# Kernel optimization log

Hardware: AMD Instinct MI355X
Metric: run time of the kernel (lower is better)

Reference implementation:

```python
import jax, jax.numpy as jnp
import numpy as np

N_NODES = 100000


def gcn_conv(x, src, dst, W, b, n_nodes):
    # PyG GCNConv: h = X W; out[i] = sum_j norm_ij * h[j] + b, with self-loops
    # and symmetric normalization norm_ij = deg(i)^-1/2 * deg(j)^-1/2.
    h = x @ W  # [N, out]
    deg = jax.ops.segment_sum(jnp.ones_like(dst, dtype=h.dtype), dst, num_segments=n_nodes)
    dinv = jnp.where(deg > 0, jax.lax.rsqrt(deg), 0.0)
    norm = dinv[src] * dinv[dst]  # [E]
    msg = h[src] * norm[:, None]  # [E, out] gather + scale
    out = jax.ops.segment_sum(msg, dst, num_segments=n_nodes)  # scatter-add
    return out + b


def setup_inputs() -> dict:
    key = jax.random.key(0)
    k_x, k_e, k_w1, k_w2 = jax.random.split(key, 4)
    in_c, hid, out_c = 128, 64, 32
    x = jax.random.normal(k_x, (N_NODES, in_c), dtype=jnp.float32)
    edge_index = jax.random.randint(k_e, (2, 1600000), 0, N_NODES, dtype=jnp.int32)
    W1 = jax.random.normal(k_w1, (in_c, hid), dtype=jnp.float32) / np.sqrt(in_c)
    b1 = jnp.zeros((hid,), dtype=jnp.float32)
    W2 = jax.random.normal(k_w2, (hid, out_c), dtype=jnp.float32) / np.sqrt(hid)
    b2 = jnp.zeros((out_c,), dtype=jnp.float32)
    return {"x": x, "edge_index": edge_index, "W1": W1, "b1": b1, "W2": W2, "b2": b2}


def reference(x, edge_index, W1, b1, W2, b2):
    n = x.shape[0]
    # add self-loops (GCNConv default)
    loops = jnp.arange(n, dtype=edge_index.dtype)
    src = jnp.concatenate([edge_index[0], loops])
    dst = jnp.concatenate([edge_index[1], loops])
    # faithful to original forward: x = (x*x)/x
    x = (x * x) / x
    h = jax.nn.relu(gcn_conv(x, src, dst, W1, b1, n))
    return gcn_conv(h, src, dst, W2, b2, n)
```

## Files before the change

### kernel.cpp

```cpp
#include <hip/hip_runtime.h>
#include <hip/hip_fp16.h>


#define IN_C 128
#define HID 64
#define OUTC 32
#define BSH 9
#define BSZ 512
#define EPB 8192

typedef _Float16 half8 __attribute__((ext_vector_type(8)));
typedef float f32x4 __attribute__((ext_vector_type(4)));

static __host__ __device__ __forceinline__ size_t szt(int a) { return (size_t)a; }

__global__ __launch_bounds__(256) void k_hist(const int* __restrict__ dst, int E,
                                              int* __restrict__ hist) {
  __shared__ int h[256];
  int tid = threadIdx.x;
  h[tid] = 0;
  __syncthreads();
  int e0 = blockIdx.x * EPB;
  int e1 = min(e0 + EPB, E);
  for (int i = e0 + tid; i < e1; i += 256) atomicAdd(&h[dst[i] >> BSH], 1);
  __syncthreads();
  hist[blockIdx.x * 256 + tid] = h[tid];
}

__global__ __launch_bounds__(256) void k_scan(int* __restrict__ hist, int B,
                                              int* __restrict__ bucket_base,
                                              int* __restrict__ bucket_count) {
  int k = threadIdx.x;
  int run = 0;
  int b = 0;
  for (; b + 4 <= B; b += 4) {
    int v0 = hist[(b + 0) * 256 + k];
    int v1 = hist[(b + 1) * 256 + k];
    int v2 = hist[(b + 2) * 256 + k];
    int v3 = hist[(b + 3) * 256 + k];
    hist[(b + 0) * 256 + k] = run; run += v0;
    hist[(b + 1) * 256 + k] = run; run += v1;
    hist[(b + 2) * 256 + k] = run; run += v2;
    hist[(b + 3) * 256 + k] = run; run += v3;
  }
  for (; b < B; ++b) {
    int v = hist[b * 256 + k];
    hist[b * 256 + k] = run;
    run += v;
  }
  __shared__ int sc[256];
  sc[k] = run;
  __syncthreads();
  for (int o = 1; o < 256; o <<= 1) {
    int v = (k >= o) ? sc[k - o] : 0;
    __syncthreads();
    sc[k] += v;
    __syncthreads();
  }
  bucket_base[k] = sc[k] - run;
  bucket_count[k] = run;
}

__global__ __launch_bounds__(256) void k_scatter(const int* __restrict__ src,
                                                 const int* __restrict__ dst, int E,
                                                 const int* __restrict__ hist,
                                                 const int* __restrict__ bucket_base,
                                                 int* __restrict__ bedges) {
  __shared__ int off[256];
  int tid = threadIdx.x;
  off[tid] = hist[blockIdx.x * 256 + tid] + bucket_base[tid];
  __syncthreads();
  int e0 = blockIdx.x * EPB;
  int e1 = min(e0 + EPB, E);
  for (int i = e0 + tid; i < e1; i += 256) {
    int d = dst[i], s = src[i];
    int p = atomicAdd(&off[d >> BSH], 1);
    bedges[p] = (s << BSH) | (d & (BSZ - 1));
  }
}

__global__ __launch_bounds__(256) void k_bucket(const int* __restrict__ bedges,
                                                const int* __restrict__ bucket_base,
                                                const int* __restrict__ bucket_count,
                                                int2* __restrict__ rd,
                                                float* __restrict__ dinv,
                                                int* __restrict__ csr, int N) {
  __shared__ int h[BSZ];
  __shared__ int pfx[BSZ];
  __shared__ int cnt[BSZ];
  __shared__ int sc[256];
  int tid = threadIdx.x;
  int b = blockIdx.x;
  int base = bucket_base[b];
  int nE = bucket_count[b];
  h[tid] = 0; h[tid + 256] = 0;
  cnt[tid] = 0; cnt[tid + 256] = 0;
  __syncthreads();
  for (int i = tid; i < nE; i += 256) atomicAdd(&h[bedges[base + i] & (BSZ - 1)], 1);
  __syncthreads();
  int a0 = h[2 * tid], a1 = h[2 * tid + 1];
  int s = a0 + a1;
  sc[tid] = s;
  __syncthreads();
  for (int o = 1; o < 256; o <<= 1) {
    int v = (tid >= o) ? sc[tid - o] : 0;
    __syncthreads();
    sc[tid] += v;
    __syncthreads();
  }
  int ex = sc[tid] - s;
  pfx[2 * tid] = ex;
  pfx[2 * tid + 1] = ex + a0;
  __syncthreads();
  for (int i = tid; i < BSZ; i += 256) {
    int node = b * BSZ + i;
    if (node < N) {
      int dg = h[i];
      rd[node] = make_int2(base + pfx[i], dg);
      dinv[node] = rsqrtf((float)(dg + 1));
    }
  }
  for (int i = tid; i < nE; i += 256) {
    int e = bedges[base + i];
    int l = e & (BSZ - 1);
    int p = pfx[l] + atomicAdd(&cnt[l], 1);
    csr[base + p] = e >> BSH;
  }
}

__global__ __launch_bounds__(256) void k_gemm1(
    const float* __restrict__ x, const float* __restrict__ W1,
    const float* __restrict__ dinv, __half* __restrict__ h1s, int N) {
  __shared__ _Float16 bf[4 * 4 * 64 * 8];
  const int tid = threadIdx.x;
  for (int idx = tid; idx < 128 * 64; idx += 256) {
    int k = idx >> 6, c = idx & 63;
    int kc = k >> 5, kk = k & 31;
    int chunk = kk >> 3, j = kk & 7;
    int ct = c >> 4, cl = c & 15;
    bf[(((kc * 4 + ct) * 64) + chunk * 16 + cl) * 8 + j] = (_Float16)W1[idx];
  }
  __syncthreads();

  const int lane = tid & 63, wave = tid >> 6;
  const int row0 = blockIdx.x * 64 + wave * 16;
  const int r_a = lane & 15;
  const int chk = lane >> 4;
  const int arow = min(row0 + r_a, N - 1);
  const float* xp = x + szt(arow) * IN_C + chk * 8;

  f32x4 acc[4];
  #pragma unroll
  for (int ct = 0; ct < 4; ++ct) acc[ct] = (f32x4){0.f, 0.f, 0.f, 0.f};

  #pragma unroll
  for (int kc = 0; kc < 4; ++kc) {
    float4 a0 = *reinterpret_cast<const float4*>(xp + kc * 32);
    float4 a1v = *reinterpret_cast<const float4*>(xp + kc * 32 + 4);
    half8 af;
    af[0] = (_Float16)a0.x;  af[1] = (_Float16)a0.y;
    af[2] = (_Float16)a0.z;  af[3] = (_Float16)a0.w;
    af[4] = (_Float16)a1v.x; af[5] = (_Float16)a1v.y;
    af[6] = (_Float16)a1v.z; af[7] = (_Float16)a1v.w;
    #pragma unroll
    for (int ct = 0; ct < 4; ++ct) {
      half8 bfrag = *reinterpret_cast<const half8*>(&bf[(((kc * 4 + ct) * 64) + lane) * 8]);
      acc[ct] = __builtin_amdgcn_mfma_f32_16x16x32_f16(af, bfrag, acc[ct], 0, 0, 0);
    }
  }
  #pragma unroll
  for (int r = 0; r < 4; ++r) {
    int drow = row0 + chk * 4 + r;
    if (drow < N) {
      float di = dinv[drow];
      #pragma unroll
      for (int ct = 0; ct < 4; ++ct)
        h1s[szt(drow) * HID + ct * 16 + r_a] = (__half)(acc[ct][r] * di);
    }
  }
}

__global__ __launch_bounds__(256) void k_agg1(
    const __half2* __restrict__ h1s2, const int* __restrict__ csr,
    const int2* __restrict__ rd, const float* __restrict__ dinv,
    const float2* __restrict__ b1f2, __half2* __restrict__ a1_2, int N) {
  int node = blockIdx.x * 8 + (threadIdx.x >> 5);
  if (node >= N) return;
  int l = threadIdx.x & 31;
  float2 acc = __half22float2(h1s2[szt(node) * 32 + l]);
  int2 v = rd[node];
  int base = v.x, cnt = v.y;
  if (cnt > 0) {
    int last = base + cnt - 1;
    int idx[8];
    #pragma unroll
    for (int u = 0; u < 8; ++u) idx[u] = csr[min(base + u, last)];
    for (int j = 0; j < cnt; j += 8) {
      __half2 g[8];
      #pragma unroll
      for (int u = 0; u < 8; ++u) g[u] = h1s2[szt(idx[u]) * 32 + l];
      int jn = j + 8;
      if (jn < cnt) {
        #pragma unroll
        for (int u = 0; u < 8; ++u) idx[u] = csr[min(base + jn + u, last)];
      }
      #pragma unroll
      for (int u = 0; u < 8; ++u) {
        float2 f = __half22float2(g[u]);
        bool ok = (j + u) < cnt;
        acc.x += ok ? f.x : 0.0f;
        acc.y += ok ? f.y : 0.0f;
      }
    }
  }
  float di = dinv[node];
  float2 bb = b1f2[l];
  float ox = fmaxf(di * acc.x + bb.x, 0.0f);
  float oy = fmaxf(di * acc.y + bb.y, 0.0f);
  a1_2[szt(node) * 32 + l] = __floats2half2_rn(ox, oy);
}

__global__ __launch_bounds__(256) void k_gemm2(
    const __half* __restrict__ a1, const float* __restrict__ W2,
    const float* __restrict__ dinv, __half* __restrict__ h2s, int N) {
  __shared__ _Float16 bf[2 * 2 * 64 * 8];
  const int tid = threadIdx.x;
  for (int idx = tid; idx < 64 * 32; idx += 256) {
    int k = idx >> 5, c = idx & 31;
    int kc = k >> 5, kk = k & 31;
    int chunk = kk >> 3, j = kk & 7;
    int ct = c >> 4, cl = c & 15;
    bf[(((kc * 2 + ct) * 64) + chunk * 16 + cl) * 8 + j] = (_Float16)W2[idx];
  }
  __syncthreads();

  const int lane = tid & 63, wave = tid >> 6;
  const int row0 = blockIdx.x * 64 + wave * 16;
  const int r_a = lane & 15;
  const int chk = lane >> 4;
  const int arow = min(row0 + r_a, N - 1);
  const _Float16* ap = (const _Float16*)a1 + szt(arow) * HID + chk * 8;

  f32x4 acc[2];
  acc[0] = (f32x4){0.f, 0.f, 0.f, 0.f};
  acc[1] = (f32x4){0.f, 0.f, 0.f, 0.f};
  #pragma unroll
  for (int kc = 0; kc < 2; ++kc) {
    half8 af = *reinterpret_cast<const half8*>(ap + kc * 32);
    #pragma unroll
    for (int ct = 0; ct < 2; ++ct) {
      half8 bfrag = *reinterpret_cast<const half8*>(&bf[(((kc * 2 + ct) * 64) + lane) * 8]);
      acc[ct] = __builtin_amdgcn_mfma_f32_16x16x32_f16(af, bfrag, acc[ct], 0, 0, 0);
    }
  }
  #pragma unroll
  for (int r = 0; r < 4; ++r) {
    int drow = row0 + chk * 4 + r;
    if (drow < N) {
      float di = dinv[drow];
      #pragma unroll
      for (int ct = 0; ct < 2; ++ct)
        h2s[szt(drow) * OUTC + ct * 16 + r_a] = (__half)(acc[ct][r] * di);
    }
  }
}

__global__ __launch_bounds__(256) void k_agg2(
    const __half2* __restrict__ h2s2, const int* __restrict__ csr,
    const int2* __restrict__ rd, const float* __restrict__ dinv,
    const float2* __restrict__ b2f2, float2* __restrict__ out2, int N) {
  int node = blockIdx.x * 16 + (threadIdx.x >> 4);
  if (node >= N) return;
  int l = threadIdx.x & 15;
  float2 acc = __half22float2(h2s2[szt(node) * 16 + l]);
  int2 v = rd[node];
  int base = v.x, cnt = v.y;
  if (cnt > 0) {
    int last = base + cnt - 1;
    int idx[8];
    #pragma unroll
    for (int u = 0; u < 8; ++u) idx[u] = csr[min(base + u, last)];
    for (int j = 0; j < cnt; j += 8) {
      __half2 g[8];
      #pragma unroll
      for (int u = 0; u < 8; ++u) g[u] = h2s2[szt(idx[u]) * 16 + l];
      int jn = j + 8;
      if (jn < cnt) {
        #pragma unroll
        for (int u = 0; u < 8; ++u) idx[u] = csr[min(base + jn + u, last)];
      }
      #pragma unroll
      for (int u = 0; u < 8; ++u) {
        float2 f = __half22float2(g[u]);
        bool ok = (j + u) < cnt;
        acc.x += ok ? f.x : 0.0f;
        acc.y += ok ? f.y : 0.0f;
      }
    }
  }
  float di = dinv[node];
  float2 bb = b2f2[l];
  out2[szt(node) * 16 + l] = make_float2(di * acc.x + bb.x, di * acc.y + bb.y);
}

extern "C" void kernel_launch(void* const* d_in, const int* in_sizes, int n_in,
                              void* d_out, int out_size, void* d_ws, size_t ws_size,
                              hipStream_t stream) {
  const float* x  = (const float*)d_in[0];
  const int*   ei = (const int*)d_in[1];
  const float* W1 = (const float*)d_in[2];
  const float* b1 = (const float*)d_in[3];
  const float* W2 = (const float*)d_in[4];
  const float* b2 = (const float*)d_in[5];
  float* out = (float*)d_out;

  const int N = in_sizes[0] / IN_C;
  const int E = in_sizes[1] / 2;
  const int* src = ei;
  const int* dst = ei + E;

  const int B  = (E + EPB - 1) / EPB;
  const int K1 = (N + BSZ - 1) / BSZ;

  char* ws = (char*)d_ws;
  size_t off = 0;
  auto alloc = [&](size_t bytes) {
    off = (off + 255) & ~(size_t)255;
    void* p = ws + off;
    off += bytes;
    return p;
  };
  int*    hist   = (int*)alloc(szt(B) * 256 * 4);
  int*    bbase  = (int*)alloc(256 * 4);
  int*    bcount = (int*)alloc(256 * 4);
  int2*   rd     = (int2*)alloc(szt(N) * 8);
  float*  dinv   = (float*)alloc(szt(N) * 4);
  int*    bedges = (int*)alloc(szt(E) * 4);
  int*    csr    = (int*)alloc(szt(E) * 4);
  __half* h1s    = (__half*)alloc(szt(N) * HID * 2);
  __half* a1     = (__half*)alloc(szt(N) * HID * 2);
  __half* h2s    = (__half*)alloc(szt(N) * OUTC * 2);
  (void)ws_size;

  k_hist<<<B, 256, 0, stream>>>(dst, E, hist);
  k_scan<<<1, 256, 0, stream>>>(hist, B, bbase, bcount);
  k_scatter<<<B, 256, 0, stream>>>(src, dst, E, hist, bbase, bedges);
  k_bucket<<<K1, 256, 0, stream>>>(bedges, bbase, bcount, rd, dinv, csr, N);
  k_gemm1<<<(N + 63) / 64, 256, 0, stream>>>(x, W1, dinv, h1s, N);
  k_agg1<<<(N + 7) / 8, 256, 0, stream>>>(
      (const __half2*)h1s, csr, rd, dinv, (const float2*)b1, (__half2*)a1, N);
  k_gemm2<<<(N + 63) / 64, 256, 0, stream>>>(a1, W2, dinv, h2s, N);
  k_agg2<<<(N + 15) / 16, 256, 0, stream>>>(
      (const __half2*)h2s, csr, rd, dinv, (const float2*)b2, (float2*)out, N);
}
```

Baseline: 139.5 us.

## Parallelize histogram scan and widen aggregation gathers to 16-byte vectors

Replaces the single-block serial column scan with a per-bucket parallel scan kernel plus a small base scan. Both aggregation kernels now use fewer lanes per node and load eight halves per lane, sharing neighbour indices across lanes with wave shuffles. The aim is to cut per-edge load instruction count and the serial scan latency. The new scan assumes at most 256 edge blocks, and the wider per-lane work raises register use.

```diff
diff --git a/kernel.cpp b/kernel.cpp
--- a/kernel.cpp
+++ b/kernel.cpp
@@ -7,6 +7,7 @@
 #define OUTC 32
 #define BSH 9
 #define BSZ 512
+#define NSLOT 256
 #define EPB 8192
 
 typedef _Float16 half8 __attribute__((ext_vector_type(8)));
@@ -16,7 +17,7 @@
 
 __global__ __launch_bounds__(256) void k_hist(const int* __restrict__ dst, int E,
                                               int* __restrict__ hist) {
-  __shared__ int h[256];
+  __shared__ int h[NSLOT];
   int tid = threadIdx.x;
   h[tid] = 0;
   __syncthreads();
@@ -24,41 +25,40 @@
   int e1 = min(e0 + EPB, E);
   for (int i = e0 + tid; i < e1; i += 256) atomicAdd(&h[dst[i] >> BSH], 1);
   __syncthreads();
-  hist[blockIdx.x * 256 + tid] = h[tid];
-}
-
-__global__ __launch_bounds__(256) void k_scan(int* __restrict__ hist, int B,
-                                              int* __restrict__ bucket_base,
-                                              int* __restrict__ bucket_count) {
-  int k = threadIdx.x;
-  int run = 0;
-  int b = 0;
-  for (; b + 4 <= B; b += 4) {
-    int v0 = hist[(b + 0) * 256 + k];
-    int v1 = hist[(b + 1) * 256 + k];
-    int v2 = hist[(b + 2) * 256 + k];
-    int v3 = hist[(b + 3) * 256 + k];
-    hist[(b + 0) * 256 + k] = run; run += v0;
-    hist[(b + 1) * 256 + k] = run; run += v1;
-    hist[(b + 2) * 256 + k] = run; run += v2;
-    hist[(b + 3) * 256 + k] = run; run += v3;
-  }
-  for (; b < B; ++b) {
-    int v = hist[b * 256 + k];
-    hist[b * 256 + k] = run;
-    run += v;
-  }
+  hist[blockIdx.x * NSLOT + tid] = h[tid];
+}
+
+__global__ __launch_bounds__(256) void k_scan_col(int* __restrict__ hist, int B,
+                                                  int* __restrict__ bucket_count) {
   __shared__ int sc[256];
-  sc[k] = run;
+  int k = blockIdx.x, t = threadIdx.x;
+  int v = (t < B) ? hist[t * NSLOT + k] : 0;
+  sc[t] = v;
   __syncthreads();
   for (int o = 1; o < 256; o <<= 1) {
-    int v = (k >= o) ? sc[k - o] : 0;
-    __syncthreads();
-    sc[k] += v;
-    __syncthreads();
-  }
-  bucket_base[k] = sc[k] - run;
-  bucket_count[k] = run;
+    int w = (t >= o) ? sc[t - o] : 0;
+    __syncthreads();
+    sc[t] += w;
+    __syncthreads();
+  }
+  if (t < B) hist[t * NSLOT + k] = sc[t] - v;
+  if (t == 255) bucket_count[k] = sc[255];
+}
+
+__global__ __launch_bounds__(256) void k_scan_base(const int* __restrict__ bucket_count,
+                                                   int* __restrict__ bucket_base) {
+  __shared__ int sc[256];
+  int t = threadIdx.x;
+  int v = bucket_count[t];
+  sc[t] = v;
+  __syncthreads();
+  for (int o = 1; o < 256; o <<= 1) {
+    int w = (t >= o) ? sc[t - o] : 0;
+    __syncthreads();
+    sc[t] += w;
+    __syncthreads();
+  }
+  bucket_base[t] = sc[t] - v;
 }
 
 __global__ __launch_bounds__(256) void k_scatter(const int* __restrict__ src,
@@ -66,9 +66,9 @@
                                                  const int* __restrict__ hist,
                                                  const int* __restrict__ bucket_base,
                                                  int* __restrict__ bedges) {
-  __shared__ int off[256];
+  __shared__ int off[NSLOT];
   int tid = threadIdx.x;
-  off[tid] = hist[blockIdx.x * 256 + tid] + bucket_base[tid];
+  off[tid] = hist[blockIdx.x * NSLOT + tid] + bucket_base[tid];
   __syncthreads();
   int e0 = blockIdx.x * EPB;
   int e1 = min(e0 + EPB, E);
@@ -181,43 +181,57 @@
 }
 
 __global__ __launch_bounds__(256) void k_agg1(
-    const __half2* __restrict__ h1s2, const int* __restrict__ csr,
+    const __half* __restrict__ h1s, const int* __restrict__ csr,
     const int2* __restrict__ rd, const float* __restrict__ dinv,
-    const float2* __restrict__ b1f2, __half2* __restrict__ a1_2, int N) {
-  int node = blockIdx.x * 8 + (threadIdx.x >> 5);
+    const float* __restrict__ b1, __half* __restrict__ a1, int N) {
+  const int tid = threadIdx.x;
+  int node = blockIdx.x * 32 + (tid >> 3);
   if (node >= N) return;
-  int l = threadIdx.x & 31;
-  float2 acc = __half22float2(h1s2[szt(node) * 32 + l]);
+  const int l = tid & 7;
+  const int g0 = (tid & 63) & ~7;
+  const _Float16* hp = (const _Float16*)h1s;
+
+  half8 selfv = *reinterpret_cast<const half8*>(hp + szt(node) * HID + l * 8);
+  float acc[8];
+  #pragma unroll
+  for (int q = 0; q < 8; ++q) acc[q] = (float)selfv[q];
+
   int2 v = rd[node];
   int base = v.x, cnt = v.y;
   if (cnt > 0) {
     int last = base + cnt - 1;
-    int idx[8];
-    #pragma unroll
-    for (int u = 0; u < 8; ++u) idx[u] = csr[min(base + u, last)];
+    int myidx = csr[min(base + l, last)];
     for (int j = 0; j < cnt; j += 8) {
-      __half2 g[8];
-      #pragma unroll
-      for (int u = 0; u < 8; ++u) g[u] = h1s2[szt(idx[u]) * 32 + l];
+      int id[8];
+      #pragma unroll
+      for (int u = 0; u < 8; ++u) id[u] = __shfl(myidx, g0 + u);
+      half8 gv[8];
+      #pragma unroll
+      for (int u = 0; u < 8; ++u)
+        gv[u] = *reinterpret_cast<const half8*>(hp + szt(id[u]) * HID + l * 8);
       int jn = j + 8;
-      if (jn < cnt) {
+      if (jn < cnt) myidx = csr[min(base + jn + l, last)];
+      #pragma unroll
+      for (int u = 0; u < 8; ++u) {
+        bool ok = (j + u) < cnt;
         #pragma unroll
-        for (int u = 0; u < 8; ++u) idx[u] = csr[min(base + jn + u, last)];
+        for (int q = 0; q < 8; ++q) acc[q] += ok ? (float)gv[u][q] : 0.0f;
       }
-      #pragma unroll
-      for (int u = 0; u < 8; ++u) {
-        float2 f = __half22float2(g[u]);
-        bool ok = (j + u) < cnt;
-        acc.x += ok ? f.x : 0.0f;
-        acc.y += ok ? f.y : 0.0f;
-      }
     }
   }
   float di = dinv[node];
-  float2 bb = b1f2[l];
-  float ox = fmaxf(di * acc.x + bb.x, 0.0f);
-  float oy = fmaxf(di * acc.y + bb.y, 0.0f);
-  a1_2[szt(node) * 32 + l] = __floats2half2_rn(ox, oy);
+  float4 bb0 = *reinterpret_cast<const float4*>(b1 + l * 8);
+  float4 bb1 = *reinterpret_cast<const float4*>(b1 + l * 8 + 4);
+  half8 o;
+  o[0] = (_Float16)fmaxf(di * acc[0] + bb0.x, 0.f);
+  o[1] = (_Float16)fmaxf(di * acc[1] + bb0.y, 0.f);
+  o[2] = (_Float16)fmaxf(di * acc[2] + bb0.z, 0.f);
+  o[3] = (_Float16)fmaxf(di * acc[3] + bb0.w, 0.f);
+  o[4] = (_Float16)fmaxf(di * acc[4] + bb1.x, 0.f);
+  o[5] = (_Float16)fmaxf(di * acc[5] + bb1.y, 0.f);
+  o[6] = (_Float16)fmaxf(di * acc[6] + bb1.z, 0.f);
+  o[7] = (_Float16)fmaxf(di * acc[7] + bb1.w, 0.f);
+  *reinterpret_cast<half8*>((_Float16*)a1 + szt(node) * HID + l * 8) = o;
 }
 
 __global__ __launch_bounds__(256) void k_gemm2(
@@ -266,41 +280,62 @@
 }
 
 __global__ __launch_bounds__(256) void k_agg2(
-    const __half2* __restrict__ h2s2, const int* __restrict__ csr,
+    const __half* __restrict__ h2s, const int* __restrict__ csr,
     const int2* __restrict__ rd, const float* __restrict__ dinv,
-    const float2* __restrict__ b2f2, float2* __restrict__ out2, int N) {
-  int node = blockIdx.x * 16 + (threadIdx.x >> 4);
+    const float* __restrict__ b2, float* __restrict__ out, int N) {
+  const int tid = threadIdx.x;
+  int node = blockIdx.x * 64 + (tid >> 2);
   if (node >= N) return;
-  int l = threadIdx.x & 15;
-  float2 acc = __half22float2(h2s2[szt(node) * 16 + l]);
+  const int l = tid & 3;
+  const int g0 = (tid & 63) & ~3;
+  const _Float16* hp = (const _Float16*)h2s;
+
+  half8 selfv = *reinterpret_cast<const half8*>(hp + szt(node) * OUTC + l * 8);
+  float acc[8];
+  #pragma unroll
+  for (int q = 0; q < 8; ++q) acc[q] = (float)selfv[q];
+
   int2 v = rd[node];
   int base = v.x, cnt = v.y;
   if (cnt > 0) {
     int last = base + cnt - 1;
-    int idx[8];
-    #pragma unroll
-    for (int u = 0; u < 8; ++u) idx[u] = csr[min(base + u, last)];
+    int myA = csr[min(base + 2 * l, last)];
+    int myB = csr[min(base + 2 * l + 1, last)];
     for (int j = 0; j < cnt; j += 8) {
-      __half2 g[8];
-      #pragma unroll
-      for (int u = 0; u < 8; ++u) g[u] = h2s2[szt(idx[u]) * 16 + l];
+      int id[8];
+      #pragma unroll
+      for (int u = 0; u < 4; ++u) {
+        id[2 * u]     = __shfl(myA, g0 + u);
+        id[2 * u + 1] = __shfl(myB, g0 + u);
+      }
+      half8 gv[8];
+      #pragma unroll
+      for (int u = 0; u < 8; ++u)
+        gv[u] = *reinterpret_cast<const half8*>(hp + szt(id[u]) * OUTC + l * 8);
       int jn = j + 8;
       if (jn < cnt) {
+        myA = csr[min(base + jn + 2 * l, last)];
+        myB = csr[min(base + jn + 2 * l + 1, last)];
+      }
+      #pragma unroll
+      for (int u = 0; u < 8; ++u) {
+        bool ok = (j + u) < cnt;
         #pragma unroll
-        for (int u = 0; u < 8; ++u) idx[u] = csr[min(base + jn + u, last)];
+        for (int q = 0; q < 8; ++q) acc[q] += ok ? (float)gv[u][q] : 0.0f;
       }
-      #pragma unroll
-      for (int u = 0; u < 8; ++u) {
-        float2 f = __half22float2(g[u]);
-        bool ok = (j + u) < cnt;
-        acc.x += ok ? f.x : 0.0f;
-        acc.y += ok ? f.y : 0.0f;
-      }
     }
   }
   float di = dinv[node];
-  float2 bb = b2f2[l];
-  out2[szt(node) * 16 + l] = make_float2(di * acc.x + bb.x, di * acc.y + bb.y);
+  float4 bb0 = *reinterpret_cast<const float4*>(b2 + l * 8);
+  float4 bb1 = *reinterpret_cast<const float4*>(b2 + l * 8 + 4);
+  float4 o0, o1;
+  o0.x = di * acc[0] + bb0.x; o0.y = di * acc[1] + bb0.y;
+  o0.z = di * acc[2] + bb0.z; o0.w = di * acc[3] + bb0.w;
+  o1.x = di * acc[4] + bb1.x; o1.y = di * acc[5] + bb1.y;
+  o1.z = di * acc[6] + bb1.z; o1.w = di * acc[7] + bb1.w;
+  float* op = out + szt(node) * OUTC + l * 8;
+  *reinterpret_cast<float4*>(op) = o0;
+  *reinterpret_cast<float4*>(op + 4) = o1;
 }
 
 extern "C" void kernel_launch(void* const* d_in, const int* in_sizes, int n_in,
@@ -330,9 +365,9 @@
     off += bytes;
     return p;
   };
-  int*    hist   = (int*)alloc(szt(B) * 256 * 4);
-  int*    bbase  = (int*)alloc(256 * 4);
-  int*    bcount = (int*)alloc(256 * 4);
+  int*    hist   = (int*)alloc(szt(B) * NSLOT * 4);
+  int*    bbase  = (int*)alloc(NSLOT * 4);
+  int*    bcount = (int*)alloc(NSLOT * 4);
   int2*   rd     = (int2*)alloc(szt(N) * 8);
   float*  dinv   = (float*)alloc(szt(N) * 4);
   int*    bedges = (int*)alloc(szt(E) * 4);
@@ -343,13 +378,12 @@
   (void)ws_size;
 
   k_hist<<<B, 256, 0, stream>>>(dst, E, hist);
-  k_scan<<<1, 256, 0, stream>>>(hist, B, bbase, bcount);
+  k_scan_col<<<NSLOT, 256, 0, stream>>>(hist, B, bcount);
+  k_scan_base<<<1, 256, 0, stream>>>(bcount, bbase);
   k_scatter<<<B, 256, 0, stream>>>(src, dst, E, hist, bbase, bedges);
   k_bucket<<<K1, 256, 0, stream>>>(bedges, bbase, bcount, rd, dinv, csr, N);
   k_gemm1<<<(N + 63) / 64, 256, 0, stream>>>(x, W1, dinv, h1s, N);
-  k_agg1<<<(N + 7) / 8, 256, 0, stream>>>(
-      (const __half2*)h1s, csr, rd, dinv, (const float2*)b1, (__half2*)a1, N);
+  k_agg1<<<(N + 31) / 32, 256, 0, stream>>>(h1s, csr, rd, dinv, b1, a1, N);
   k_gemm2<<<(N + 63) / 64, 256, 0, stream>>>(a1, W2, dinv, h2s, N);
-  k_agg2<<<(N + 15) / 16, 256, 0, stream>>>(
-      (const __half2*)h2s, csr, rd, dinv, (const float2*)b2, (float2*)out, N);
-}
+  k_agg2<<<(N + 63) / 64, 256, 0, stream>>>(h2s, csr, rd, dinv, b2, out, N);
+}
```

Measured after the change: 127.4 us. -8.6%, faster.
